# Kernel tuning notes

Hardware: AMD Instinct MI355X
Metric: run time of the kernel (lower is better)

The kernel has to match this reference:

```python
import jax, jax.numpy as jnp
import numpy as np

B, S, D = 2, 2048, 2048
H, DK, DV, L = 16, 128, 128, 64


def setup_inputs() -> dict:
    key = jax.random.key(0)
    ks = jax.random.split(key, 12)
    s = lambda k, shape, fan_in: jax.random.normal(k, shape, jnp.float32) / np.sqrt(fan_in)
    return {
        "queries": jax.random.normal(ks[0], (B, S, D), jnp.float32),
        "keys": jax.random.normal(ks[1], (B, S, D), jnp.float32),
        "values": jax.random.normal(ks[2], (B, S, D), jnp.float32),
        "Wq": s(ks[3], (D, H * DK), D), "bq": jnp.zeros((H * DK,), jnp.float32),
        "Wlk": s(ks[4], (D, H * L), D), "blk": jnp.zeros((H * L,), jnp.float32),
        "Wlv": s(ks[5], (D, H * L), D), "blv": jnp.zeros((H * L,), jnp.float32),
        "Wkr": s(ks[6], (L, DK), L),
        "Wvr": s(ks[7], (L, DV), L),
        "Wout": s(ks[8], (H * DV, D), H * DV), "bout": jnp.zeros((D,), jnp.float32),
    }


def reference(queries, keys, values, Wq, bq, Wlk, blk, Wlv, blv, Wkr, Wvr, Wout, bout):
    b, sq, _ = queries.shape
    sk = keys.shape[1]
    # projections -> [b, h, s, d]
    q = (queries @ Wq + bq).reshape(b, sq, H, DK).transpose(0, 2, 1, 3)
    lk = (keys @ Wlk + blk).reshape(b, sk, H, L).transpose(0, 2, 1, 3)
    lv = (values @ Wlv + blv).reshape(b, sk, H, L).transpose(0, 2, 1, 3)
    k = lk @ Wkr  # [b,h,sk,DK] latent -> key reconstruction
    v = lv @ Wvr  # [b,h,sk,DV]
    scores = jnp.einsum('bhqd,bhkd->bhqk', q, k) / np.sqrt(DK).astype(np.float32)
    causal = jnp.triu(jnp.ones((sq, sk), dtype=bool), k=1)
    scores = jnp.where(causal, -jnp.inf, scores)
    attn = jax.nn.softmax(scores, axis=-1)
    out = jnp.einsum('bhqk,bhkd->bhqd', attn, v)
    out = out.transpose(0, 2, 1, 3).reshape(b, sq, H * DV)
    return out @ Wout + bout
```

## Files before the change

kernel.cpp:

```cpp
#include <hip/hip_runtime.h>
#include <cstdint>
#include <cstddef>

typedef _Float16 f16;
typedef __attribute__((ext_vector_type(8))) _Float16 f16x8;
typedef __attribute__((ext_vector_type(4))) _Float16 f16x4;
typedef __attribute__((ext_vector_type(4))) float f32x4;

constexpr int kB  = 2;
constexpr int kS  = 2048;
constexpr int kD  = 2048;
constexpr int kH  = 16;
constexpr int kL  = 64;
constexpr int kHL = kH * kL;
constexpr int kBS = kB * kS;

__device__ __forceinline__ void load_lds16(const void* g, void* l) {
  __builtin_amdgcn_global_load_lds((const __attribute__((address_space(1))) void*)g,
                                   (__attribute__((address_space(3))) void*)l, 16, 0, 0);
}

__device__ __forceinline__ f32x4 mfma16(f16x8 a, f16x8 b, f32x4 c) {
  return __builtin_amdgcn_mfma_f32_16x16x32_f16(a, b, c, 0, 0, 0);
}


__global__ void cast4(const float* __restrict__ a, const float* __restrict__ b,
                      const float* __restrict__ c, const float* __restrict__ d,
                      f16* __restrict__ oa, f16* __restrict__ ob,
                      f16* __restrict__ oc, f16* __restrict__ od) {
  const int z = blockIdx.z;
  int i = blockIdx.x * 256 + threadIdx.x;
  if (z == 3 && i >= kD * kD / 4) return;
  const float* in = z == 0 ? a : z == 1 ? b : z == 2 ? c : d;
  f16* out = z == 0 ? oa : z == 1 ? ob : z == 2 ? oc : od;
  float4 f = ((const float4*)in)[i];
  f16x4 o; o[0] = (f16)f.x; o[1] = (f16)f.y; o[2] = (f16)f.z; o[3] = (f16)f.w;
  ((f16x4*)out)[i] = o;
}

__device__ __forceinline__ void transpose_body(const float* __restrict__ in,
                                               f16* __restrict__ out, int R, int C) {
  const int r0 = blockIdx.y * 64, c0 = blockIdx.x * 64;
  __shared__ float tile[64][65];
  const int t = threadIdx.x;
  const int cc = t & 63, rr = t >> 6;
#pragma unroll
  for (int p = 0; p < 16; p++) {
    int r = p * 4 + rr;
    tile[r][cc] = in[(size_t)(r0 + r) * C + c0 + cc];
  }
  __syncthreads();
#pragma unroll
  for (int p = 0; p < 16; p++) {
    int c = p * 4 + rr;
    out[(size_t)(c0 + c) * R + r0 + cc] = (f16)tile[cc][c];
  }
}

__global__ __launch_bounds__(256) void transpose3(const float* __restrict__ Wlk,
                                                  const float* __restrict__ Wlv,
                                                  const float* __restrict__ Wout,
                                                  f16* __restrict__ Wlkt,
                                                  f16* __restrict__ Wlvt,
                                                  f16* __restrict__ WoutT) {
  const int z = blockIdx.z;
  if (z < 2 && blockIdx.x >= 16) return;
  if (z == 0) transpose_body(Wlk, Wlkt, 2048, 1024);
  else if (z == 1) transpose_body(Wlv, Wlvt, 2048, 1024);
  else transpose_body(Wout, WoutT, 2048, 2048);
}

__global__ void fold_bq(const float* __restrict__ bq, const float* __restrict__ Wkr,
                        float* __restrict__ bql) {
  int hl = blockIdx.x * 256 + threadIdx.x;
  if (hl >= kHL) return;
  int h = hl >> 6, l = hl & 63;
  float s = 0.f;
  for (int c = 0; c < 128; c++) s += bq[h * 128 + c] * Wkr[l * 128 + c];
  bql[hl] = s;
}

__global__ __launch_bounds__(256) void fold2(const float* __restrict__ Wkr,
                                             const float* __restrict__ Wvr,
                                             const f16* __restrict__ Wq16,
                                             const f16* __restrict__ WoutT,
                                             f16* __restrict__ Wqlt,
                                             f16* __restrict__ W2t) {
  __shared__ f16 sA[64 * 136];
  __shared__ f16 sB[128 * 128];
  const int z = blockIdx.z;
  const int h = blockIdx.y;
  const int d0 = blockIdx.x * 128;
  const float* Wsm = z ? Wvr : Wkr;
  const f16* Bsrc = (z ? WoutT : Wq16) + h * 128;
  const int tid = threadIdx.x;
  const int w = tid >> 6, lane = tid & 63;
  const int quad = lane >> 4, l16 = lane & 15;

#pragma unroll
  for (int it = 0; it < 8; it++) {
    int i = it * 256 + tid;
    float4 f = ((const float4*)Wsm)[i];
    int e = i * 4, r = e >> 7, c = e & 127;
    f16x4 o; o[0] = (f16)f.x; o[1] = (f16)f.y; o[2] = (f16)f.z; o[3] = (f16)f.w;
    *(f16x4*)&sA[r * 136 + c] = o;
  }
#pragma unroll
  for (int c = 0; c < 8; c++) {
    int rbase = w * 32 + c * 4;
    load_lds16(Bsrc + (size_t)(d0 + rbase + (lane >> 4)) * 2048 + (lane & 15) * 8,
               &sB[rbase * 128]);
  }
  __syncthreads();

  if (z == 0) {
    f32x4 acc[4][2];
    for (int mt = 0; mt < 4; mt++)
      for (int nt = 0; nt < 2; nt++) acc[mt][nt] = (f32x4){0.f, 0.f, 0.f, 0.f};
#pragma unroll
    for (int ks = 0; ks < 4; ks++) {
      f16x8 af[4], bf[2];
#pragma unroll
      for (int mt = 0; mt < 4; mt++)
        af[mt] = *(const f16x8*)&sA[(mt * 16 + l16) * 136 + ks * 32 + quad * 8];
#pragma unroll
      for (int nt = 0; nt < 2; nt++)
        bf[nt] = *(const f16x8*)&sB[(w * 32 + nt * 16 + l16) * 128 + ks * 32 + quad * 8];
#pragma unroll
      for (int mt = 0; mt < 4; mt++)
#pragma unroll
        for (int nt = 0; nt < 2; nt++) acc[mt][nt] = mfma16(af[mt], bf[nt], acc[mt][nt]);
    }
#pragma unroll
    for (int mt = 0; mt < 4; mt++)
#pragma unroll
      for (int nt = 0; nt < 2; nt++)
#pragma unroll
        for (int r = 0; r < 4; r++) {
          int row = mt * 16 + quad * 4 + r;
          int col = d0 + w * 32 + nt * 16 + l16;
          Wqlt[(size_t)(h * 64 + row) * 2048 + col] = (f16)acc[mt][nt][r];
        }
  } else {
    f32x4 acc[2][4];
    for (int mt = 0; mt < 2; mt++)
      for (int nt = 0; nt < 4; nt++) acc[mt][nt] = (f32x4){0.f, 0.f, 0.f, 0.f};
#pragma unroll
    for (int ks = 0; ks < 4; ks++) {
      f16x8 af[2], bf[4];
#pragma unroll
      for (int mt = 0; mt < 2; mt++)
        af[mt] = *(const f16x8*)&sB[(w * 32 + mt * 16 + l16) * 128 + ks * 32 + quad * 8];
#pragma unroll
      for (int nt = 0; nt < 4; nt++)
        bf[nt] = *(const f16x8*)&sA[(nt * 16 + l16) * 136 + ks * 32 + quad * 8];
#pragma unroll
      for (int mt = 0; mt < 2; mt++)
#pragma unroll
        for (int nt = 0; nt < 4; nt++) acc[mt][nt] = mfma16(af[mt], bf[nt], acc[mt][nt]);
    }
#pragma unroll
    for (int mt = 0; mt < 2; mt++)
#pragma unroll
      for (int nt = 0; nt < 4; nt++)
#pragma unroll
        for (int r = 0; r < 4; r++) {
          int row = d0 + w * 32 + mt * 16 + quad * 4 + r;
          int col = nt * 16 + l16;
          W2t[(size_t)row * 1024 + h * 64 + col] = (f16)acc[mt][nt][r];
        }
  }
}

template <typename OutT, bool HAS_BIAS>
__device__ __forceinline__ void gemm_body(const f16* __restrict__ A, const f16* __restrict__ Bt,
                                          const float* __restrict__ bias, OutT* __restrict__ C,
                                          int N, int K) {
  __shared__ f16 sA[128 * 64];
  __shared__ f16 sB[128 * 64];
  const int tid = threadIdx.x;
  const int w = tid >> 6, lane = tid & 63;
  const int quad = lane >> 4, l16 = lane & 15;
  const int wm = w >> 1, wn = w & 1;
  const int m0 = blockIdx.y * 128, n0 = blockIdx.x * 128;
  const int rowA = lane >> 3;
  const int colSw = (((lane & 7) ^ (lane >> 3)) << 3) ;
  const int sw0 = ((quad ^ (l16 & 7)) << 3);
  const int sw1 = (((4 + quad) ^ (l16 & 7)) << 3);

  f32x4 acc[4][4];
  for (int i = 0; i < 4; i++)
    for (int j = 0; j < 4; j++) acc[i][j] = (f32x4){0.f, 0.f, 0.f, 0.f};

  for (int k0 = 0; k0 < K; k0 += 64) {
    __syncthreads();
#pragma unroll
    for (int c = 0; c < 4; c++) {
      int rl = w * 32 + c * 8;
      load_lds16(A + (size_t)(m0 + rl + rowA) * K + k0 + colSw, &sA[rl * 64]);
      load_lds16(Bt + (size_t)(n0 + rl + rowA) * K + k0 + colSw, &sB[rl * 64]);
    }
    __syncthreads();
#pragma unroll
    for (int ks = 0; ks < 2; ks++) {
      const int sw = ks ? sw1 : sw0;
      f16x8 af[4], bfr[4];
#pragma unroll
      for (int mt = 0; mt < 4; mt++)
        af[mt] = *(const f16x8*)&sA[(wm * 64 + mt * 16 + l16) * 64 + sw];
#pragma unroll
      for (int nt = 0; nt < 4; nt++)
        bfr[nt] = *(const f16x8*)&sB[(wn * 64 + nt * 16 + l16) * 64 + sw];
#pragma unroll
      for (int mt = 0; mt < 4; mt++) {
#pragma unroll
        for (int nt = 0; nt < 4; nt++)
          acc[mt][nt] = mfma16(af[mt], bfr[nt], acc[mt][nt]);
      }
    }
  }
#pragma unroll
  for (int mt = 0; mt < 4; mt++) {
#pragma unroll
    for (int nt = 0; nt < 4; nt++) {
      int col = n0 + wn * 64 + nt * 16 + l16;
      float bv = HAS_BIAS ? bias[col] : 0.f;
#pragma unroll
      for (int r = 0; r < 4; r++) {
        int row = m0 + wm * 64 + mt * 16 + quad * 4 + r;
        C[(size_t)row * N + col] = (OutT)(acc[mt][nt][r] + bv);
      }
    }
  }
}

__global__ __launch_bounds__(256) void gemm3_f16(
    const f16* __restrict__ A0, const f16* __restrict__ A1, const f16* __restrict__ A2,
    const f16* __restrict__ B0, const f16* __restrict__ B1, const f16* __restrict__ B2,
    const float* __restrict__ c0, const float* __restrict__ c1, const float* __restrict__ c2,
    f16* __restrict__ C0, f16* __restrict__ C1, f16* __restrict__ C2, int N, int K) {
  const f16* A = blockIdx.z == 0 ? A0 : blockIdx.z == 1 ? A1 : A2;
  const f16* Bt = blockIdx.z == 0 ? B0 : blockIdx.z == 1 ? B1 : B2;
  const float* bias = blockIdx.z == 0 ? c0 : blockIdx.z == 1 ? c1 : c2;
  f16* C = blockIdx.z == 0 ? C0 : blockIdx.z == 1 ? C1 : C2;
  gemm_body<f16, true>(A, Bt, bias, C, N, K);
}

__global__ __launch_bounds__(256) void gemm_f32(const f16* __restrict__ A,
                                                const f16* __restrict__ Bt,
                                                const float* __restrict__ bias,
                                                float* __restrict__ C, int N, int K) {
  gemm_body<float, true>(A, Bt, bias, C, N, K);
}

__global__ __launch_bounds__(256) void transpose_lv(const f16* __restrict__ LV,
                                                    f16* __restrict__ LVt) {
  const int bh = blockIdx.y, b = bh >> 4, h = bh & 15;
  const int s0 = blockIdx.x * 64;
  __shared__ f16 tile[64][65];
  const int t = threadIdx.x;
  const int c0 = t & 63, r0 = t >> 6;
#pragma unroll
  for (int r = 0; r < 16; r++) {
    int s = r * 4 + r0;
    tile[s][c0] = LV[(size_t)(b * kS + s0 + s) * kHL + h * kL + c0];
  }
  __syncthreads();
#pragma unroll
  for (int r = 0; r < 16; r++) {
    int vl = r * 4 + r0;
    LVt[((size_t)bh * kL + vl) * kS + s0 + c0] = tile[c0][vl];
  }
}

__global__ __launch_bounds__(256) void attn(const f16* __restrict__ Qlat,
                                            const f16* __restrict__ LK,
                                            const f16* __restrict__ LVt,
                                            f16* __restrict__ Ctx) {
  const int bh = blockIdx.y, b = bh >> 4, h = bh & 15;
  const int pair = blockIdx.x;
  const int tid = threadIdx.x;
  const int w = tid >> 6, lane = tid & 63;
  const int quad = lane >> 4, l16 = lane & 15;

  __shared__ f16 sK[64 * 64];
  __shared__ f16 sV[64 * 64];
  __shared__ f16 sP[4][16 * 72];

  const f16* qbase = Qlat + (size_t)b * kS * kHL + h * kL;
  const f16* kbase = LK + (size_t)b * kS * kHL + h * kL;
  const f16* vbase = LVt + (size_t)bh * kL * kS;

  const float scale = 0.08838834764831845f;
  const int rowA = lane >> 3;
  const int colSw = (((lane & 7) ^ (lane >> 3)) << 3);
  const int sw0 = ((quad ^ (l16 & 7)) << 3);
  const int sw1 = (((4 + quad) ^ (l16 & 7)) << 3);

#pragma unroll
  for (int which = 0; which < 2; which++) {
    const int t = which ? (31 - pair) : pair;
    const int q0 = t * 64;
    const int qrow = q0 + w * 16 + l16;

    f16x8 aq[2];
#pragma unroll
    for (int ks = 0; ks < 2; ks++)
      aq[ks] = *(const f16x8*)(qbase + (size_t)qrow * kHL + ks * 32 + quad * 8);

    f32x4 acc[4];
    for (int nt = 0; nt < 4; nt++) acc[nt] = (f32x4){0.f, 0.f, 0.f, 0.f};
    float mst[4], lst[4];
    for (int r = 0; r < 4; r++) { mst[r] = -3.0e38f; lst[r] = 0.f; }

    for (int kv0 = 0; kv0 <= q0; kv0 += 64) {
      __syncthreads();
#pragma unroll
      for (int c = 0; c < 2; c++) {
        int rl = w * 16 + c * 8;
        load_lds16(kbase + (size_t)(kv0 + rl + rowA) * kHL + colSw, &sK[rl * 64]);
        load_lds16(vbase + (size_t)(rl + rowA) * kS + kv0 + colSw, &sV[rl * 64]);
      }
      __syncthreads();

      f32x4 sc[4];
      for (int nt = 0; nt < 4; nt++) sc[nt] = (f32x4){0.f, 0.f, 0.f, 0.f};
#pragma unroll
      for (int ks = 0; ks < 2; ks++) {
        const int sw = ks ? sw1 : sw0;
        f16x8 bk[4];
#pragma unroll
        for (int nt = 0; nt < 4; nt++)
          bk[nt] = *(const f16x8*)&sK[(nt * 16 + l16) * 64 + sw];
#pragma unroll
        for (int nt = 0; nt < 4; nt++) sc[nt] = mfma16(aq[ks], bk[nt], sc[nt]);
      }

      float tmax[4] = {-3.0e38f, -3.0e38f, -3.0e38f, -3.0e38f};
      if (kv0 == q0) {
#pragma unroll
        for (int nt = 0; nt < 4; nt++) {
          int kvg = kv0 + nt * 16 + l16;
#pragma unroll
          for (int r = 0; r < 4; r++) {
            int qg = q0 + w * 16 + quad * 4 + r;
            float s = sc[nt][r] * scale;
            if (kvg > qg) s = -1.0e30f;
            sc[nt][r] = s;
            tmax[r] = fmaxf(tmax[r], s);
          }
        }
      } else {
#pragma unroll
        for (int nt = 0; nt < 4; nt++) {
#pragma unroll
          for (int r = 0; r < 4; r++) {
            float s = sc[nt][r] * scale;
            sc[nt][r] = s;
            tmax[r] = fmaxf(tmax[r], s);
          }
        }
      }
#pragma unroll
      for (int r = 0; r < 4; r++) {
        float tm = tmax[r];
        tm = fmaxf(tm, __shfl_xor(tm, 1));
        tm = fmaxf(tm, __shfl_xor(tm, 2));
        tm = fmaxf(tm, __shfl_xor(tm, 4));
        tm = fmaxf(tm, __shfl_xor(tm, 8));
        tmax[r] = tm;
      }
      float alpha[4], psum[4];
#pragma unroll
      for (int r = 0; r < 4; r++) {
        float mnew = fmaxf(mst[r], tmax[r]);
        alpha[r] = __expf(mst[r] - mnew);
        mst[r] = mnew;
        psum[r] = 0.f;
      }
#pragma unroll
      for (int nt = 0; nt < 4; nt++) {
#pragma unroll
        for (int r = 0; r < 4; r++) {
          float p = __expf(sc[nt][r] - mst[r]);
          psum[r] += p;
          sP[w][(quad * 4 + r) * 72 + nt * 16 + l16] = (f16)p;
        }
      }
#pragma unroll
      for (int r = 0; r < 4; r++) {
        float s = psum[r];
        s += __shfl_xor(s, 1);
        s += __shfl_xor(s, 2);
        s += __shfl_xor(s, 4);
        s += __shfl_xor(s, 8);
        lst[r] = lst[r] * alpha[r] + s;
      }
#pragma unroll
      for (int nt = 0; nt < 4; nt++) {
#pragma unroll
        for (int r = 0; r < 4; r++) acc[nt][r] *= alpha[r];
      }

#pragma unroll
      for (int ks = 0; ks < 2; ks++) {
        const int sw = ks ? sw1 : sw0;
        f16x8 ap = *(const f16x8*)&sP[w][l16 * 72 + ks * 32 + quad * 8];
        f16x8 bv[4];
#pragma unroll
        for (int nt = 0; nt < 4; nt++)
          bv[nt] = *(const f16x8*)&sV[(nt * 16 + l16) * 64 + sw];
#pragma unroll
        for (int nt = 0; nt < 4; nt++) acc[nt] = mfma16(ap, bv[nt], acc[nt]);
      }
    }

#pragma unroll
    for (int r = 0; r < 4; r++) {
      float inv = 1.f / lst[r];
      int qg = q0 + w * 16 + quad * 4 + r;
      size_t base = (size_t)(b * kS + qg) * kHL + h * kL;
#pragma unroll
      for (int nt = 0; nt < 4; nt++)
        Ctx[base + nt * 16 + l16] = (f16)(acc[nt][r] * inv);
    }
  }
}

extern "C" void kernel_launch(void* const* d_in, const int* in_sizes, int n_in,
                              void* d_out, int out_size, void* d_ws, size_t ws_size,
                              hipStream_t stream) {
  (void)in_sizes; (void)n_in; (void)out_size; (void)ws_size;
  const float* queries = (const float*)d_in[0];
  const float* keys    = (const float*)d_in[1];
  const float* values  = (const float*)d_in[2];
  const float* Wq      = (const float*)d_in[3];
  const float* bq      = (const float*)d_in[4];
  const float* Wlk     = (const float*)d_in[5];
  const float* blk     = (const float*)d_in[6];
  const float* Wlv     = (const float*)d_in[7];
  const float* blv     = (const float*)d_in[8];
  const float* Wkr     = (const float*)d_in[9];
  const float* Wvr     = (const float*)d_in[10];
  const float* Wout    = (const float*)d_in[11];
  const float* bout    = (const float*)d_in[12];

  char* ws = (char*)d_ws;
  size_t off = 0;
  auto alloc = [&](size_t bytes) {
    void* p = ws + off;
    off += (bytes + 255) & ~(size_t)255;
    return p;
  };
  f16* qb    = (f16*)alloc((size_t)kBS * kD * 2);
  f16* kb    = (f16*)alloc((size_t)kBS * kD * 2);
  f16* vb    = (f16*)alloc((size_t)kBS * kD * 2);
  f16* Wqlt  = (f16*)alloc((size_t)kHL * kD * 2);
  f16* Wlkt  = (f16*)alloc((size_t)kHL * kD * 2);
  f16* Wlvt  = (f16*)alloc((size_t)kHL * kD * 2);
  f16* W2t   = (f16*)alloc((size_t)kD * kHL * 2);
  float* bql = (float*)alloc(kHL * 4);
  f16* Qlat  = (f16*)alloc((size_t)kBS * kHL * 2);
  f16* LKb   = (f16*)alloc((size_t)kBS * kHL * 2);
  f16* LVb   = (f16*)alloc((size_t)kBS * kHL * 2);
  f16* Wq16  = Qlat;
  f16* WoutT = LKb;
  f16* LVtb = qb;
  f16* Ctx  = kb;

  const int n4 = kBS * kD / 4;
  cast4<<<dim3(n4 / 256, 1, 4), 256, 0, stream>>>(queries, keys, values, Wq, qb, kb, vb, Wq16);
  transpose3<<<dim3(32, 32, 3), 256, 0, stream>>>(Wlk, Wlv, Wout, Wlkt, Wlvt, WoutT);
  fold_bq<<<kHL / 256, 256, 0, stream>>>(bq, Wkr, bql);
  fold2<<<dim3(16, 16, 2), 256, 0, stream>>>(Wkr, Wvr, Wq16, WoutT, Wqlt, W2t);

  gemm3_f16<<<dim3(kHL / 128, kBS / 128, 3), 256, 0, stream>>>(
      qb, kb, vb, Wqlt, Wlkt, Wlvt, bql, blk, blv, Qlat, LKb, LVb, kHL, kD);

  transpose_lv<<<dim3(kS / 64, kB * kH), 256, 0, stream>>>(LVb, LVtb);
  attn<<<dim3(16, kB * kH), 256, 0, stream>>>(Qlat, LKb, LVtb, Ctx);
  gemm_f32<<<dim3(kD / 128, kBS / 128), 256, 0, stream>>>(Ctx, W2t, bout, (float*)d_out, kD, kHL);
}
```

Measured before the change: 381.1 us.

## Double-buffer K/V tiles and restructure softmax with transposed scores

The attention kernel now double-buffers the K and V LDS tiles, prefetching the next tile while computing on the current one, which drops one barrier per iteration. The score MFMA operands are swapped so each lane owns a single query row. That turns the per-row max and sum reductions into two cross-quad shuffles and allows packed f16x4 stores of P. Softmax uses exp2 with a folded scale and skips the accumulator rescale when no row max grows, at the cost of double the K/V LDS footprint and a possible occupancy drop.

```diff
diff --git a/kernel.cpp b/kernel.cpp
--- a/kernel.cpp
+++ b/kernel.cpp
@@ -284,25 +284,26 @@
   const int w = tid >> 6, lane = tid & 63;
   const int quad = lane >> 4, l16 = lane & 15;
 
-  __shared__ f16 sK[64 * 64];
-  __shared__ f16 sV[64 * 64];
+  __shared__ f16 sK[2][64 * 64];
+  __shared__ f16 sV[2][64 * 64];
   __shared__ f16 sP[4][16 * 72];
 
   const f16* qbase = Qlat + (size_t)b * kS * kHL + h * kL;
   const f16* kbase = LK + (size_t)b * kS * kHL + h * kL;
   const f16* vbase = LVt + (size_t)bh * kL * kS;
 
-  const float scale = 0.08838834764831845f;
+  const float cscale = 0.08838834764831845f * 1.4426950408889634f;
   const int rowA = lane >> 3;
   const int colSw = (((lane & 7) ^ (lane >> 3)) << 3);
   const int sw0 = ((quad ^ (l16 & 7)) << 3);
   const int sw1 = (((4 + quad) ^ (l16 & 7)) << 3);
 
-#pragma unroll
   for (int which = 0; which < 2; which++) {
     const int t = which ? (31 - pair) : pair;
     const int q0 = t * 64;
     const int qrow = q0 + w * 16 + l16;
+    const int qg = qrow;
+    const int ntile = t + 1;
 
     f16x8 aq[2];
 #pragma unroll
@@ -311,18 +312,35 @@
 
     f32x4 acc[4];
     for (int nt = 0; nt < 4; nt++) acc[nt] = (f32x4){0.f, 0.f, 0.f, 0.f};
-    float mst[4], lst[4];
-    for (int r = 0; r < 4; r++) { mst[r] = -3.0e38f; lst[r] = 0.f; }
-
-    for (int kv0 = 0; kv0 <= q0; kv0 += 64) {
+    float m_s = -3.0e38f;
+    float l_part = 0.f;
+
+    __syncthreads();
+    {
+      const int rl = w * 16;
+      load_lds16(kbase + (size_t)(rl + rowA) * kHL + colSw, &sK[0][rl * 64]);
+      load_lds16(vbase + (size_t)(rl + rowA) * kS + colSw, &sV[0][rl * 64]);
+      load_lds16(kbase + (size_t)(rl + 8 + rowA) * kHL + colSw, &sK[0][(rl + 8) * 64]);
+      load_lds16(vbase + (size_t)(rl + 8 + rowA) * kS + colSw, &sV[0][(rl + 8) * 64]);
+    }
+    int cur = 0;
+
+    for (int it = 0; it < ntile; ++it) {
+      const int kv0 = it * 64;
       __syncthreads();
-#pragma unroll
-      for (int c = 0; c < 2; c++) {
-        int rl = w * 16 + c * 8;
-        load_lds16(kbase + (size_t)(kv0 + rl + rowA) * kHL + colSw, &sK[rl * 64]);
-        load_lds16(vbase + (size_t)(rl + rowA) * kS + kv0 + colSw, &sV[rl * 64]);
-      }
-      __syncthreads();
+
+      if (it + 1 < ntile) {
+        const int nkv = kv0 + 64;
+        f16* dK = &sK[cur ^ 1][0];
+        f16* dV = &sV[cur ^ 1][0];
+        const int rl = w * 16;
+        load_lds16(kbase + (size_t)(nkv + rl + rowA) * kHL + colSw, dK + rl * 64);
+        load_lds16(vbase + (size_t)(rl + rowA) * kS + nkv + colSw, dV + rl * 64);
+        load_lds16(kbase + (size_t)(nkv + rl + 8 + rowA) * kHL + colSw, dK + (rl + 8) * 64);
+        load_lds16(vbase + (size_t)(rl + 8 + rowA) * kS + nkv + colSw, dV + (rl + 8) * 64);
+      }
+      const f16* sKc = &sK[cur][0];
+      const f16* sVc = &sV[cur][0];
 
       f32x4 sc[4];
       for (int nt = 0; nt < 4; nt++) sc[nt] = (f32x4){0.f, 0.f, 0.f, 0.f};
@@ -332,76 +350,57 @@
         f16x8 bk[4];
 #pragma unroll
         for (int nt = 0; nt < 4; nt++)
-          bk[nt] = *(const f16x8*)&sK[(nt * 16 + l16) * 64 + sw];
-#pragma unroll
-        for (int nt = 0; nt < 4; nt++) sc[nt] = mfma16(aq[ks], bk[nt], sc[nt]);
-      }
-
-      float tmax[4] = {-3.0e38f, -3.0e38f, -3.0e38f, -3.0e38f};
+          bk[nt] = *(const f16x8*)&sKc[(nt * 16 + l16) * 64 + sw];
+#pragma unroll
+        for (int nt = 0; nt < 4; nt++) sc[nt] = mfma16(bk[nt], aq[ks], sc[nt]);
+      }
+
       if (kv0 == q0) {
 #pragma unroll
         for (int nt = 0; nt < 4; nt++) {
-          int kvg = kv0 + nt * 16 + l16;
 #pragma unroll
           for (int r = 0; r < 4; r++) {
-            int qg = q0 + w * 16 + quad * 4 + r;
-            float s = sc[nt][r] * scale;
-            if (kvg > qg) s = -1.0e30f;
-            sc[nt][r] = s;
-            tmax[r] = fmaxf(tmax[r], s);
+            int kvg = kv0 + nt * 16 + quad * 4 + r;
+            if (kvg > qg) sc[nt][r] = -1.0e30f;
           }
         }
-      } else {
-#pragma unroll
-        for (int nt = 0; nt < 4; nt++) {
-#pragma unroll
-          for (int r = 0; r < 4; r++) {
-            float s = sc[nt][r] * scale;
-            sc[nt][r] = s;
-            tmax[r] = fmaxf(tmax[r], s);
-          }
+      }
+
+      float tm = -3.0e38f;
+#pragma unroll
+      for (int nt = 0; nt < 4; nt++)
+        tm = fmaxf(tm, fmaxf(fmaxf(sc[nt][0], sc[nt][1]), fmaxf(sc[nt][2], sc[nt][3])));
+      tm = fmaxf(tm, __shfl_xor(tm, 16));
+      tm = fmaxf(tm, __shfl_xor(tm, 32));
+      const float tms = tm * cscale;
+
+      if (!__all(tms <= m_s)) {
+        const float mnew = fmaxf(m_s, tms);
+        const float alpha = __builtin_amdgcn_exp2f(m_s - mnew);
+        m_s = mnew;
+        l_part *= alpha;
+        float ar[4];
+#pragma unroll
+        for (int r = 0; r < 4; r++) ar[r] = __shfl(alpha, quad * 4 + r);
+#pragma unroll
+        for (int nt = 0; nt < 4; nt++)
+#pragma unroll
+          for (int r = 0; r < 4; r++) acc[nt][r] *= ar[r];
+      }
+
+      float ps = 0.f;
+#pragma unroll
+      for (int nt = 0; nt < 4; nt++) {
+        f16x4 pk;
+#pragma unroll
+        for (int r = 0; r < 4; r++) {
+          float p = __builtin_amdgcn_exp2f(__builtin_fmaf(sc[nt][r], cscale, -m_s));
+          ps += p;
+          pk[r] = (f16)p;
         }
-      }
-#pragma unroll
-      for (int r = 0; r < 4; r++) {
-        float tm = tmax[r];
-        tm = fmaxf(tm, __shfl_xor(tm, 1));
-        tm = fmaxf(tm, __shfl_xor(tm, 2));
-        tm = fmaxf(tm, __shfl_xor(tm, 4));
-        tm = fmaxf(tm, __shfl_xor(tm, 8));
-        tmax[r] = tm;
-      }
-      float alpha[4], psum[4];
-#pragma unroll
-      for (int r = 0; r < 4; r++) {
-        float mnew = fmaxf(mst[r], tmax[r]);
-        alpha[r] = __expf(mst[r] - mnew);
-        mst[r] = mnew;
-        psum[r] = 0.f;
-      }
-#pragma unroll
-      for (int nt = 0; nt < 4; nt++) {
-#pragma unroll
-        for (int r = 0; r < 4; r++) {
-          float p = __expf(sc[nt][r] - mst[r]);
-          psum[r] += p;
-          sP[w][(quad * 4 + r) * 72 + nt * 16 + l16] = (f16)p;
-        }
-      }
-#pragma unroll
-      for (int r = 0; r < 4; r++) {
-        float s = psum[r];
-        s += __shfl_xor(s, 1);
-        s += __shfl_xor(s, 2);
-        s += __shfl_xor(s, 4);
-        s += __shfl_xor(s, 8);
-        lst[r] = lst[r] * alpha[r] + s;
-      }
-#pragma unroll
-      for (int nt = 0; nt < 4; nt++) {
-#pragma unroll
-        for (int r = 0; r < 4; r++) acc[nt][r] *= alpha[r];
-      }
+        *(f16x4*)&sP[w][l16 * 72 + nt * 16 + quad * 4] = pk;
+      }
+      l_part += ps;
 
 #pragma unroll
       for (int ks = 0; ks < 2; ks++) {
@@ -410,20 +409,26 @@
         f16x8 bv[4];
 #pragma unroll
         for (int nt = 0; nt < 4; nt++)
-          bv[nt] = *(const f16x8*)&sV[(nt * 16 + l16) * 64 + sw];
+          bv[nt] = *(const f16x8*)&sVc[(nt * 16 + l16) * 64 + sw];
 #pragma unroll
         for (int nt = 0; nt < 4; nt++) acc[nt] = mfma16(ap, bv[nt], acc[nt]);
       }
-    }
-
+      cur ^= 1;
+    }
+
+    float lfull = l_part;
+    lfull += __shfl_xor(lfull, 16);
+    lfull += __shfl_xor(lfull, 32);
+    float inv[4];
+#pragma unroll
+    for (int r = 0; r < 4; r++) inv[r] = 1.f / __shfl(lfull, quad * 4 + r);
 #pragma unroll
     for (int r = 0; r < 4; r++) {
-      float inv = 1.f / lst[r];
-      int qg = q0 + w * 16 + quad * 4 + r;
-      size_t base = (size_t)(b * kS + qg) * kHL + h * kL;
+      int qout = q0 + w * 16 + quad * 4 + r;
+      size_t base = (size_t)(b * kS + qout) * kHL + h * kL;
 #pragma unroll
       for (int nt = 0; nt < 4; nt++)
-        Ctx[base + nt * 16 + l16] = (f16)(acc[nt][r] * inv);
+        Ctx[base + nt * 16 + l16] = (f16)(acc[nt][r] * inv[r]);
     }
   }
 }
```

Result: faster. 371.9 us (-2.4%).
